# Kernel tuning notes

Measured on AMD Instinct MI355X. Metric: run time of the kernel, lower is better.

The kernel has to match this reference:

```python
import jax, jax.numpy as jnp
import numpy as np
import math

C = 768; H = 12; B = 2; TX = 2048; TC = 2048

def setup_inputs() -> dict:
    key = jax.random.key(0)
    ks = jax.random.split(key, 20)
    w = lambda k, s: jax.random.normal(k, s, dtype=jnp.float32) * 0.02
    inp = {
        "x": jax.random.normal(ks[0], (B, TX, C), dtype=jnp.float32),
        "context": jax.random.normal(ks[1], (B, TC, C), dtype=jnp.float32),
        "ln1_g": jnp.ones((C,), jnp.float32), "ln1_b": jnp.zeros((C,), jnp.float32),
        "ln2_g": jnp.ones((C,), jnp.float32), "ln2_b": jnp.zeros((C,), jnp.float32),
        "ln3_g": jnp.ones((C,), jnp.float32), "ln3_b": jnp.zeros((C,), jnp.float32),
        "sa_wq": w(ks[2], (C, C)), "sa_bq": jnp.zeros((C,), jnp.float32),
        "sa_wk": w(ks[3], (C, C)), "sa_bk": jnp.zeros((C,), jnp.float32),
        "sa_wv": w(ks[4], (C, C)), "sa_bv": jnp.zeros((C,), jnp.float32),
        "sa_wo": w(ks[5], (C, C)), "sa_bo": jnp.zeros((C,), jnp.float32),
        "xa_wq": w(ks[6], (C, C)), "xa_bq": jnp.zeros((C,), jnp.float32),
        "xa_wk": w(ks[7], (C, C)), "xa_bk": jnp.zeros((C,), jnp.float32),
        "xa_wv": w(ks[8], (C, C)), "xa_bv": jnp.zeros((C,), jnp.float32),
        "xa_wo": w(ks[9], (C, C)), "xa_bo": jnp.zeros((C,), jnp.float32),
        "mlp_w1": w(ks[10], (C, 4 * C)), "mlp_b1": jnp.zeros((4 * C,), jnp.float32),
        "mlp_w2": w(ks[11], (4 * C, C)), "mlp_b2": jnp.zeros((C,), jnp.float32),
        "n_head": H,
    }
    return inp

def _layernorm(x, g, b, eps=1e-5):
    mu = jnp.mean(x, axis=-1, keepdims=True)
    var = jnp.mean(jnp.square(x - mu), axis=-1, keepdims=True)
    return (x - mu) * jax.lax.rsqrt(var + eps) * g + b

def _attn(xq, xkv, wq, bq, wk, bk, wv, bv, wo, bo, n_head):
    Bq, Tq, Cm = xq.shape
    Tk = xkv.shape[1]
    dh = Cm // n_head
    q = (xq @ wq + bq).reshape(Bq, Tq, n_head, dh)
    k = (xkv @ wk + bk).reshape(Bq, Tk, n_head, dh)
    v = (xkv @ wv + bv).reshape(Bq, Tk, n_head, dh)
    att = jnp.einsum('bqhd,bkhd->bhqk', q, k) * (1.0 / math.sqrt(dh))
    att = jax.nn.softmax(att, axis=-1)
    y = jnp.einsum('bhqk,bkhd->bqhd', att, v).reshape(Bq, Tq, Cm)
    return y @ wo + bo

def reference(x, context, ln1_g, ln1_b, ln2_g, ln2_b, ln3_g, ln3_b,
              sa_wq, sa_bq, sa_wk, sa_bk, sa_wv, sa_bv, sa_wo, sa_bo,
              xa_wq, xa_bq, xa_wk, xa_bk, xa_wv, xa_bv, xa_wo, xa_bo,
              mlp_w1, mlp_b1, mlp_w2, mlp_b2, n_head):
    # pre-LN residual self-attention
    x = x + _attn(_layernorm(x, ln1_g, ln1_b), _layernorm(x, ln1_g, ln1_b),
                  sa_wq, sa_bq, sa_wk, sa_bk, sa_wv, sa_bv, sa_wo, sa_bo, n_head)
    # pre-LN residual cross-attention (context not normalized, matching source)
    x = x + _attn(_layernorm(x, ln2_g, ln2_b), context,
                  xa_wq, xa_bq, xa_wk, xa_bk, xa_wv, xa_bv, xa_wo, xa_bo, n_head)
    # pre-LN residual MLP with exact (erf) GELU, as torch.nn.GELU default
    h = _layernorm(x, ln3_g, ln3_b)
    x = x + (jax.nn.gelu(h @ mlp_w1 + mlp_b1, approximate=False) @ mlp_w2 + mlp_b2)
    return (x, context)
```

## Files before the change

kernel.cpp:

```cpp
#include <hip/hip_runtime.h>
#include <hip/hip_bf16.h>
#include <math.h>

#define CDIM 768
#define HDIM 3072
#define NROWS 4096
#define TSEQ 2048
#define NHEAD 12
#define KVSPLIT 4
#define KVLEN (TSEQ / KVSPLIT)

typedef unsigned short u16;
typedef unsigned int   u32;
typedef __attribute__((ext_vector_type(8))) short short8;
typedef __attribute__((ext_vector_type(4))) float f32x4;

#define QSCALE 0.18033688011112042f

static __device__ __forceinline__ u16 f2bf(float f) {
    u32 x = __float_as_uint(f);
    x += 0x7fffu + ((x >> 16) & 1u);
    return (u16)(x >> 16);
}
static __device__ __forceinline__ float bf2f(u16 x) {
    return __uint_as_float((u32)x << 16);
}
static __device__ __forceinline__ u32 cvt_pk_bf16(float lo, float hi) {
    u32 r;
    asm("v_cvt_pk_bf16_f32 %0, %1, %2" : "=v"(r) : "v"(lo), "v"(hi));
    return r;
}

#define GLL16(g, l)                                                            \
    __builtin_amdgcn_global_load_lds(                                          \
        (const __attribute__((address_space(1))) void*)(g),                    \
        (__attribute__((address_space(3))) void*)(l), 16, 0, 0)

__launch_bounds__(256)
__global__ void wtrans(const float* __restrict__ w, u16* __restrict__ wt,
                       int K, int N) {
    __shared__ float t[32][33];
    const int n0 = blockIdx.x * 32, k0 = blockIdx.y * 32;
    const int tx = threadIdx.x & 31, ty = threadIdx.x >> 5;
#pragma unroll
    for (int i = ty; i < 32; i += 8)
        t[i][tx] = w[(size_t)(k0 + i) * N + n0 + tx];
    __syncthreads();
#pragma unroll
    for (int i = ty; i < 32; i += 8)
        wt[(size_t)(n0 + i) * K + k0 + tx] = f2bf(t[tx][i]);
}

struct WT4 { const float* w[4]; u16* wt[4]; };
__launch_bounds__(256)
__global__ void wtrans4(WT4 a) {
    __shared__ float t[32][33];
    const float* __restrict__ w = a.w[blockIdx.z];
    u16* __restrict__ wt = a.wt[blockIdx.z];
    const int n0 = blockIdx.x * 32, k0 = blockIdx.y * 32;
    const int tx = threadIdx.x & 31, ty = threadIdx.x >> 5;
#pragma unroll
    for (int i = ty; i < 32; i += 8)
        t[i][tx] = w[(size_t)(k0 + i) * CDIM + n0 + tx];
    __syncthreads();
#pragma unroll
    for (int i = ty; i < 32; i += 8)
        wt[(size_t)(n0 + i) * CDIM + k0 + tx] = f2bf(t[tx][i]);
}

__launch_bounds__(256)
__global__ void cvt_copy(const float* __restrict__ in, u16* __restrict__ out,
                         int n4) {
    int i = blockIdx.x * 256 + threadIdx.x;
    if (i >= n4) return;
    float4 v = ((const float4*)in)[i];
    ushort4 o;
    o.x = f2bf(v.x); o.y = f2bf(v.y); o.z = f2bf(v.z); o.w = f2bf(v.w);
    ((ushort4*)out)[i] = o;
}

__launch_bounds__(256)
__global__ void ln_kernel(const float* __restrict__ x, const float* __restrict__ g,
                          const float* __restrict__ bta, u16* __restrict__ out) {
    const int row = blockIdx.x, tid = threadIdx.x;
    const float* xr = x + (size_t)row * CDIM;
    float v0 = xr[tid], v1 = xr[tid + 256], v2 = xr[tid + 512];
    __shared__ float red[8];
    float s = v0 + v1 + v2;
#pragma unroll
    for (int m = 1; m < 64; m <<= 1) s += __shfl_xor(s, m);
    if ((tid & 63) == 0) red[tid >> 6] = s;
    __syncthreads();
    const float mu = (red[0] + red[1] + red[2] + red[3]) * (1.f / CDIM);
    const float d0 = v0 - mu, d1 = v1 - mu, d2 = v2 - mu;
    float q = d0 * d0 + d1 * d1 + d2 * d2;
#pragma unroll
    for (int m = 1; m < 64; m <<= 1) q += __shfl_xor(q, m);
    if ((tid & 63) == 0) red[4 + (tid >> 6)] = q;
    __syncthreads();
    const float var = (red[4] + red[5] + red[6] + red[7]) * (1.f / CDIM);
    const float rstd = rsqrtf(var + 1e-5f);
    u16* orow = out + (size_t)row * CDIM;
    orow[tid]       = f2bf(d0 * rstd * g[tid]       + bta[tid]);
    orow[tid + 256] = f2bf(d1 * rstd * g[tid + 256] + bta[tid + 256]);
    orow[tid + 512] = f2bf(d2 * rstd * g[tid + 512] + bta[tid + 512]);
}

struct GemmArgs {
    const u16* A[3];
    const u16* BT[3];
    const float* bias[3];
    const float* res[3];
    void* out[3];
    float alpha[3];
    int M, N, K;
};

template <int EPI, int BM, int BN = 128>
__launch_bounds__(256)
__global__ void gemm_bt(GemmArgs ga) {
    constexpr int MF = BM / 32, NF = BN / 32;
    __shared__ u16 Abuf[BM * 32];
    __shared__ u16 Bbuf[BN * 32];
    const int z = blockIdx.z;
    const u16* __restrict__ A  = ga.A[z];
    const u16* __restrict__ BT = ga.BT[z];
    const float* __restrict__ bias = ga.bias[z];
    const float* __restrict__ res  = ga.res[z];
    void* outv = ga.out[z];
    const float alpha = ga.alpha[z];
    const int N = ga.N, K = ga.K;

    const int tid = threadIdx.x;
    const int lane = tid & 63, w = tid >> 6;
    const int m0 = blockIdx.x * BM, n0 = blockIdx.y * BN;
    const int wr = (w >> 1) * (BM / 2), wc = (w & 1) * (BN / 2);
    const int lr = lane & 15, lc = lane >> 4;

    const int srowA = (BM == 128) ? (w * 32 + (lane >> 2)) : (tid >> 2);
    const int srowB = (BN == 128) ? (w * 32 + (lane >> 2)) : (tid >> 2);
    const int scol = (lane & 3) * 8;
    const u16* Ag = A + (size_t)(m0 + srowA) * K + scol;
    const u16* Bg = BT + (size_t)(n0 + srowB) * K + scol;
    char* Ab = (char*)Abuf + w * (BM == 128 ? 2048 : 1024);
    char* Bb = (char*)Bbuf + w * (BN == 128 ? 2048 : 1024);

    f32x4 acc[MF][NF];
#pragma unroll
    for (int m = 0; m < MF; ++m)
#pragma unroll
        for (int n = 0; n < NF; ++n) acc[m][n] = (f32x4){0.f, 0.f, 0.f, 0.f};

    const int nk = K >> 5;
    for (int kt = 0; kt < nk; ++kt) {
        const int ko = kt * 32;
        GLL16(Ag + ko, Ab);
        if constexpr (BM == 128) GLL16(Ag + 16 * K + ko, Ab + 1024);
        GLL16(Bg + ko, Bb);
        if constexpr (BN == 128) GLL16(Bg + 16 * K + ko, Bb + 1024);
        __syncthreads();
        short8 af[MF], bfv[NF];
#pragma unroll
        for (int m = 0; m < MF; ++m)
            af[m] = *(const short8*)((const char*)Abuf +
                                     (size_t)(wr + m * 16 + lr) * 64 + lc * 16);
#pragma unroll
        for (int n = 0; n < NF; ++n)
            bfv[n] = *(const short8*)((const char*)Bbuf +
                                      (size_t)(wc + n * 16 + lr) * 64 + lc * 16);
#pragma unroll
        for (int m = 0; m < MF; ++m)
#pragma unroll
            for (int n = 0; n < NF; ++n)
                acc[m][n] = __builtin_amdgcn_mfma_f32_16x16x32_bf16(
                    af[m], bfv[n], acc[m][n], 0, 0, 0);
        __syncthreads();
    }

#pragma unroll
    for (int n = 0; n < NF; ++n) {
        const int gc = n0 + wc + n * 16 + lr;
        const float bs = bias[gc];
#pragma unroll
        for (int m = 0; m < MF; ++m) {
            const int gr = m0 + wr + m * 16 + lc * 4;
#pragma unroll
            for (int r = 0; r < 4; ++r) {
                float v = (acc[m][n][r] + bs) * alpha;
                const size_t idx = (size_t)(gr + r) * N + gc;
                if constexpr (EPI == 0) {
                    ((u16*)outv)[idx] = f2bf(v);
                } else if constexpr (EPI == 1) {
                    ((float*)outv)[idx] = res[idx] + v;
                } else {
                    float gel = 0.5f * v * (1.0f + erff(v * 0.70710678118654752f));
                    ((u16*)outv)[idx] = f2bf(gel);
                }
            }
        }
    }
}

static __device__ __forceinline__ void softmax_pack(f32x4 sf[4], float& mrow,
                                                    float& lrow, f32x4 oacc[4],
                                                    short8& p0, short8& p1) {
    float pm;
    {
        float a0 = fmaxf(fmaxf(sf[0][0], sf[0][1]), fmaxf(sf[0][2], sf[0][3]));
        float a1 = fmaxf(fmaxf(sf[1][0], sf[1][1]), fmaxf(sf[1][2], sf[1][3]));
        float a2 = fmaxf(fmaxf(sf[2][0], sf[2][1]), fmaxf(sf[2][2], sf[2][3]));
        float a3 = fmaxf(fmaxf(sf[3][0], sf[3][1]), fmaxf(sf[3][2], sf[3][3]));
        pm = fmaxf(fmaxf(a0, a1), fmaxf(a2, a3));
        pm = fmaxf(pm, __shfl_xor(pm, 16));
        pm = fmaxf(pm, __shfl_xor(pm, 32));
    }
    if (!__all(pm <= mrow)) {
        const float mn = fmaxf(mrow, pm);
        const float corr = exp2f(mrow - mn);
        mrow = mn;
        lrow *= corr;
#pragma unroll
        for (int fd = 0; fd < 4; ++fd)
#pragma unroll
            for (int r = 0; r < 4; ++r) oacc[fd][r] *= corr;
    }
#pragma unroll
    for (int fn = 0; fn < 4; ++fn)
#pragma unroll
        for (int r = 0; r < 4; ++r) sf[fn][r] = exp2f(sf[fn][r] - mrow);
    float rs;
    {
        float s0 = (sf[0][0] + sf[0][1]) + (sf[0][2] + sf[0][3]);
        float s1 = (sf[1][0] + sf[1][1]) + (sf[1][2] + sf[1][3]);
        float s2 = (sf[2][0] + sf[2][1]) + (sf[2][2] + sf[2][3]);
        float s3 = (sf[3][0] + sf[3][1]) + (sf[3][2] + sf[3][3]);
        rs = (s0 + s1) + (s2 + s3);
        rs += __shfl_xor(rs, 16);
        rs += __shfl_xor(rs, 32);
    }
    lrow += rs;
    int4 pw0, pw1;
    pw0.x = cvt_pk_bf16(sf[0][0], sf[0][1]);
    pw0.y = cvt_pk_bf16(sf[0][2], sf[0][3]);
    pw0.z = cvt_pk_bf16(sf[1][0], sf[1][1]);
    pw0.w = cvt_pk_bf16(sf[1][2], sf[1][3]);
    pw1.x = cvt_pk_bf16(sf[2][0], sf[2][1]);
    pw1.y = cvt_pk_bf16(sf[2][2], sf[2][3]);
    pw1.z = cvt_pk_bf16(sf[3][0], sf[3][1]);
    pw1.w = cvt_pk_bf16(sf[3][2], sf[3][3]);
    p0 = *(short8*)&pw0;
    p1 = *(short8*)&pw1;
}

__launch_bounds__(256, 4)
__global__ void attn_split(const u16* __restrict__ Qb, const u16* __restrict__ Kb,
                           const u16* __restrict__ Vb, u16* __restrict__ Opart,
                           float2* __restrict__ ml) {
    __shared__ u16 Klds[64 * 72];
    __shared__ u16 Vt[64 * 72];
    const int tid = threadIdx.x;
    const int lane = tid & 63, w = tid >> 6;
    const int lr = lane & 15, lc = lane >> 4;
    const int b = blockIdx.y / NHEAD, h = blockIdx.y % NHEAD;
    const int z = blockIdx.z;
    const size_t qrowA = (size_t)b * TSEQ + blockIdx.x * 128 + w * 16;
    const size_t qrowB = qrowA + 64;
    const size_t krow0 = (size_t)b * TSEQ + (size_t)z * KVLEN;
    const int hc = h * 64;

    short8 qa0, qa1, qb0, qb1;
    {
        const u16* qp = Qb + (qrowA + lr) * CDIM + hc + lc * 8;
        qa0 = *(const short8*)qp;
        qa1 = *(const short8*)(qp + 32);
        const u16* qp2 = Qb + (qrowB + lr) * CDIM + hc + lc * 8;
        qb0 = *(const short8*)qp2;
        qb1 = *(const short8*)(qp2 + 32);
    }
    f32x4 oaccA[4], oaccB[4];
#pragma unroll
    for (int r = 0; r < 4; ++r) {
        oaccA[r] = (f32x4){0.f, 0.f, 0.f, 0.f};
        oaccB[r] = (f32x4){0.f, 0.f, 0.f, 0.f};
    }
    float mA = -3e38f, lA = 0.f, mB = -3e38f, lB = 0.f;

    const int stg_r = tid >> 2, stg_s = tid & 3;
    const u16* kg = Kb + (krow0 + stg_r) * CDIM + hc + stg_s * 16;
    const u16* vg = Vb + (krow0 + stg_r) * CDIM + hc + stg_s * 16;
    uint4 ka0 = *(const uint4*)kg, ka1 = *(const uint4*)(kg + 8);
    uint4 va0 = *(const uint4*)vg, va1 = *(const uint4*)(vg + 8);
    const int sig = ((stg_r >> 5) << 5) + (((stg_r >> 2) & 3) << 3) +
                    (((stg_r >> 4) & 1) << 2) + (stg_r & 3);
    char* vdst = (char*)Vt + ((2 * sig) ^ (stg_s << 5)) +
                 (size_t)(stg_s * 16) * 144;

    for (int kt = 0; kt < KVLEN / 64; ++kt) {
        __syncthreads();
        {
            *(uint4*)&Klds[stg_r * 72 + stg_s * 16]     = ka0;
            *(uint4*)&Klds[stg_r * 72 + stg_s * 16 + 8] = ka1;
            u16 tmp[16];
            *(uint4*)(tmp)     = va0;
            *(uint4*)(tmp + 8) = va1;
#pragma unroll
            for (int j = 0; j < 16; ++j)
                *(u16*)(vdst + (size_t)j * 144) = tmp[j];
        }
        if (kt < KVLEN / 64 - 1) {
            kg += 64 * CDIM; vg += 64 * CDIM;
            ka0 = *(const uint4*)kg; ka1 = *(const uint4*)(kg + 8);
            va0 = *(const uint4*)vg; va1 = *(const uint4*)(vg + 8);
        }
        __syncthreads();

        f32x4 sfA[4], sfB[4];
#pragma unroll
        for (int fn = 0; fn < 4; ++fn) {
            const u16* kr = &Klds[(lr + fn * 16) * 72 + lc * 8];
            short8 kb0 = *(const short8*)kr;
            short8 kb1 = *(const short8*)(kr + 32);
            f32x4 t = (f32x4){0.f, 0.f, 0.f, 0.f};
            t = __builtin_amdgcn_mfma_f32_16x16x32_bf16(kb0, qa0, t, 0, 0, 0);
            t = __builtin_amdgcn_mfma_f32_16x16x32_bf16(kb1, qa1, t, 0, 0, 0);
            sfA[fn] = t;
            f32x4 u = (f32x4){0.f, 0.f, 0.f, 0.f};
            u = __builtin_amdgcn_mfma_f32_16x16x32_bf16(kb0, qb0, u, 0, 0, 0);
            u = __builtin_amdgcn_mfma_f32_16x16x32_bf16(kb1, qb1, u, 0, 0, 0);
            sfB[fn] = u;
        }

        short8 pA0, pA1, pB0, pB1;
        softmax_pack(sfA, mA, lA, oaccA, pA0, pA1);
        softmax_pack(sfB, mB, lB, oaccB, pB0, pB1);

#pragma unroll
        for (int fd = 0; fd < 4; ++fd) {
            const char* vtb = (const char*)Vt + (size_t)(lr + fd * 16) * 144;
            short8 vb0 = *(const short8*)(vtb + ((lc * 16) ^ (fd * 32)));
            short8 vb1 = *(const short8*)(vtb + ((lc * 16 + 64) ^ (fd * 32)));
            oaccA[fd] = __builtin_amdgcn_mfma_f32_16x16x32_bf16(vb0, pA0, oaccA[fd], 0, 0, 0);
            oaccA[fd] = __builtin_amdgcn_mfma_f32_16x16x32_bf16(vb1, pA1, oaccA[fd], 0, 0, 0);
            oaccB[fd] = __builtin_amdgcn_mfma_f32_16x16x32_bf16(vb0, pB0, oaccB[fd], 0, 0, 0);
            oaccB[fd] = __builtin_amdgcn_mfma_f32_16x16x32_bf16(vb1, pB1, oaccB[fd], 0, 0, 0);
        }
    }

    u16* oA = Opart + (size_t)z * NROWS * CDIM + (qrowA + lr) * CDIM + hc + lc * 4;
    u16* oB = Opart + (size_t)z * NROWS * CDIM + (qrowB + lr) * CDIM + hc + lc * 4;
#pragma unroll
    for (int fd = 0; fd < 4; ++fd) {
        ushort4 o;
        o.x = f2bf(oaccA[fd][0]); o.y = f2bf(oaccA[fd][1]);
        o.z = f2bf(oaccA[fd][2]); o.w = f2bf(oaccA[fd][3]);
        *(ushort4*)(oA + fd * 16) = o;
        o.x = f2bf(oaccB[fd][0]); o.y = f2bf(oaccB[fd][1]);
        o.z = f2bf(oaccB[fd][2]); o.w = f2bf(oaccB[fd][3]);
        *(ushort4*)(oB + fd * 16) = o;
    }
    if (lc == 0) {
        ml[((size_t)z * NROWS + qrowA + lr) * NHEAD + h] = (float2){mA, lA};
        ml[((size_t)z * NROWS + qrowB + lr) * NHEAD + h] = (float2){mB, lB};
    }
}

__launch_bounds__(256)
__global__ void attn_merge4(const u16* __restrict__ P, const float2* __restrict__ ml,
                            u16* __restrict__ out) {
    const int i4 = blockIdx.x * 256 + threadIdx.x;
    const size_t base = (size_t)i4 * 4;
    const int row = (int)(base / CDIM);
    const int head = (int)(base - (size_t)row * CDIM) >> 6;
    float2 a[KVSPLIT];
    float M = -3e38f;
#pragma unroll
    for (int z = 0; z < KVSPLIT; ++z) {
        a[z] = ml[((size_t)z * NROWS + row) * NHEAD + head];
        M = fmaxf(M, a[z].x);
    }
    float den = 0.f, e[KVSPLIT];
#pragma unroll
    for (int z = 0; z < KVSPLIT; ++z) {
        e[z] = exp2f(a[z].x - M);
        den += a[z].y * e[z];
    }
    const float rden = 1.f / den;
    float o0 = 0.f, o1 = 0.f, o2 = 0.f, o3 = 0.f;
#pragma unroll
    for (int z = 0; z < KVSPLIT; ++z) {
        ushort4 p = *(const ushort4*)(P + (size_t)z * NROWS * CDIM + base);
        o0 += bf2f(p.x) * e[z];
        o1 += bf2f(p.y) * e[z];
        o2 += bf2f(p.z) * e[z];
        o3 += bf2f(p.w) * e[z];
    }
    ushort4 o;
    o.x = f2bf(o0 * rden); o.y = f2bf(o1 * rden);
    o.z = f2bf(o2 * rden); o.w = f2bf(o3 * rden);
    *(ushort4*)(out + base) = o;
}

extern "C" void kernel_launch(void* const* d_in, const int* in_sizes, int n_in,
                              void* d_out, int out_size, void* d_ws, size_t ws_size,
                              hipStream_t stream) {
    const float* x     = (const float*)d_in[0];
    const float* ctx   = (const float*)d_in[1];
    const float* ln1g  = (const float*)d_in[2];
    const float* ln1b  = (const float*)d_in[3];
    const float* ln2g  = (const float*)d_in[4];
    const float* ln2b  = (const float*)d_in[5];
    const float* ln3g  = (const float*)d_in[6];
    const float* ln3b  = (const float*)d_in[7];
    const float* sa_wq = (const float*)d_in[8];
    const float* sa_bq = (const float*)d_in[9];
    const float* sa_wk = (const float*)d_in[10];
    const float* sa_bk = (const float*)d_in[11];
    const float* sa_wv = (const float*)d_in[12];
    const float* sa_bv = (const float*)d_in[13];
    const float* sa_wo = (const float*)d_in[14];
    const float* sa_bo = (const float*)d_in[15];
    const float* xa_wq = (const float*)d_in[16];
    const float* xa_bq = (const float*)d_in[17];
    const float* xa_wk = (const float*)d_in[18];
    const float* xa_bk = (const float*)d_in[19];
    const float* xa_wv = (const float*)d_in[20];
    const float* xa_bv = (const float*)d_in[21];
    const float* xa_wo = (const float*)d_in[22];
    const float* xa_bo = (const float*)d_in[23];
    const float* m_w1  = (const float*)d_in[24];
    const float* m_b1  = (const float*)d_in[25];
    const float* m_w2  = (const float*)d_in[26];
    const float* m_b2  = (const float*)d_in[27];

    float* out_x   = (float*)d_out;
    float* out_ctx = out_x + (size_t)NROWS * CDIM;
    u16* Opart = (u16*)d_out;

    const size_t SZ_ACT  = (size_t)NROWS * CDIM * 2;
    const size_t SZ_WBIG = (size_t)HDIM * CDIM * 2;
    const size_t SZ_R    = (size_t)NROWS * CDIM * 4;
    const size_t NEEDED  = 5 * SZ_ACT + SZ_R + SZ_WBIG;
    if (ws_size < NEEDED) return;

    char* ws = (char*)d_ws;
    u16* qb    = (u16*)(ws);
    u16* kb    = (u16*)(ws + 1 * SZ_ACT);
    u16* vb    = (u16*)(ws + 2 * SZ_ACT);
    u16* ctxb  = (u16*)(ws + 3 * SZ_ACT);
    u16* hb    = qb;
    u16* lnbuf = (u16*)(ws + 4 * SZ_ACT);
    u16* attB  = lnbuf;
    float* R   = (float*)(ws + 5 * SZ_ACT);
    u16* Wq    = (u16*)(ws + 5 * SZ_ACT + SZ_R);
    u16* Wk    = Wq + (size_t)CDIM * CDIM;
    u16* Wv    = Wk + (size_t)CDIM * CDIM;
    u16* Wo    = Wv + (size_t)CDIM * CDIM;
    float2* ml = (float2*)Wq;

    const dim3 tb(256);
    GemmArgs ga;
    WT4 wg;

    cvt_copy<<<dim3(3072), tb, 0, stream>>>(ctx, ctxb, NROWS * CDIM / 4);

    ln_kernel<<<dim3(NROWS), tb, 0, stream>>>(x, ln1g, ln1b, lnbuf);
    wg.w[0] = sa_wq; wg.w[1] = sa_wk; wg.w[2] = sa_wv; wg.w[3] = sa_wo;
    wg.wt[0] = Wq;   wg.wt[1] = Wk;   wg.wt[2] = Wv;   wg.wt[3] = Wo;
    wtrans4<<<dim3(24, 24, 4), tb, 0, stream>>>(wg);
    ga = GemmArgs{};
    ga.A[0] = lnbuf; ga.BT[0] = Wq; ga.bias[0] = sa_bq; ga.out[0] = qb; ga.alpha[0] = QSCALE;
    ga.A[1] = lnbuf; ga.BT[1] = Wk; ga.bias[1] = sa_bk; ga.out[1] = kb; ga.alpha[1] = 1.f;
    ga.A[2] = lnbuf; ga.BT[2] = Wv; ga.bias[2] = sa_bv; ga.out[2] = vb; ga.alpha[2] = 1.f;
    ga.M = 4096; ga.N = 768; ga.K = 768;
    gemm_bt<0, 128><<<dim3(32, 6, 3), tb, 0, stream>>>(ga);
    attn_split<<<dim3(16, 24, KVSPLIT), tb, 0, stream>>>(qb, kb, vb, Opart, ml);
    attn_merge4<<<dim3(NROWS * CDIM / 1024), tb, 0, stream>>>(Opart, ml, attB);
    ga = GemmArgs{};
    ga.A[0] = attB; ga.BT[0] = Wo; ga.bias[0] = sa_bo; ga.res[0] = x; ga.out[0] = R; ga.alpha[0] = 1.f;
    ga.M = 4096; ga.N = 768; ga.K = 768;
    gemm_bt<1, 64, 64><<<dim3(64, 12, 1), tb, 0, stream>>>(ga);

    ln_kernel<<<dim3(NROWS), tb, 0, stream>>>(R, ln2g, ln2b, lnbuf);
    wg.w[0] = xa_wq; wg.w[1] = xa_wk; wg.w[2] = xa_wv; wg.w[3] = xa_wo;
    wg.wt[0] = Wq;   wg.wt[1] = Wk;   wg.wt[2] = Wv;   wg.wt[3] = Wo;
    wtrans4<<<dim3(24, 24, 4), tb, 0, stream>>>(wg);
    ga = GemmArgs{};
    ga.A[0] = lnbuf; ga.BT[0] = Wq; ga.bias[0] = xa_bq; ga.out[0] = qb; ga.alpha[0] = QSCALE;
    ga.A[1] = ctxb;  ga.BT[1] = Wk; ga.bias[1] = xa_bk; ga.out[1] = kb; ga.alpha[1] = 1.f;
    ga.A[2] = ctxb;  ga.BT[2] = Wv; ga.bias[2] = xa_bv; ga.out[2] = vb; ga.alpha[2] = 1.f;
    ga.M = 4096; ga.N = 768; ga.K = 768;
    gemm_bt<0, 128><<<dim3(32, 6, 3), tb, 0, stream>>>(ga);
    attn_split<<<dim3(16, 24, KVSPLIT), tb, 0, stream>>>(qb, kb, vb, Opart, ml);
    attn_merge4<<<dim3(NROWS * CDIM / 1024), tb, 0, stream>>>(Opart, ml, attB);
    hipMemcpyAsync(out_ctx, ctx, (size_t)NROWS * CDIM * 4,
                   hipMemcpyDeviceToDevice, stream);
    ga = GemmArgs{};
    ga.A[0] = attB; ga.BT[0] = Wo; ga.bias[0] = xa_bo; ga.res[0] = R; ga.out[0] = R; ga.alpha[0] = 1.f;
    ga.M = 4096; ga.N = 768; ga.K = 768;
    gemm_bt<1, 64, 64><<<dim3(64, 12, 1), tb, 0, stream>>>(ga);

    ln_kernel<<<dim3(NROWS), tb, 0, stream>>>(R, ln3g, ln3b, lnbuf);
    wtrans<<<dim3(96, 24), tb, 0, stream>>>(m_w1, Wq, 768, 3072);
    ga = GemmArgs{};
    ga.A[0] = lnbuf; ga.BT[0] = Wq; ga.bias[0] = m_b1; ga.out[0] = hb; ga.alpha[0] = 1.f;
    ga.M = 4096; ga.N = 3072; ga.K = 768;
    gemm_bt<2, 128><<<dim3(32, 24, 1), tb, 0, stream>>>(ga);
    wtrans<<<dim3(24, 96), tb, 0, stream>>>(m_w2, Wq, 3072, 768);
    ga = GemmArgs{};
    ga.A[0] = hb; ga.BT[0] = Wq; ga.bias[0] = m_b2; ga.res[0] = R; ga.out[0] = out_x; ga.alpha[0] = 1.f;
    ga.M = 4096; ga.N = 768; ga.K = 3072;
    gemm_bt<1, 64, 64><<<dim3(64, 12, 1), tb, 0, stream>>>(ga);

    (void)in_sizes; (void)n_in; (void)out_size;
}
```

Baseline: 340.7 us.

## Merge layernorm, conversions and weight transposes into combined prologue kernels

Replaces the separate cvt_copy, ln_kernel and weight-transpose launches before each stage with one kernel per stage that dispatches on block index, which removes several launches and lets the independent pieces overlap. The W2 transpose now goes to the output context area as scratch, so it can be done up front, and the context memcpy moves to the very end. The QKV GEMMs also switch to a narrower 128x64 tile with twice as many blocks. Costs are branch divergence across block roles and reuse of the output buffer as scratch before the final copy.

```diff
diff --git a/kernel.cpp b/kernel.cpp
--- a/kernel.cpp
+++ b/kernel.cpp
@@ -36,56 +36,22 @@
         (const __attribute__((address_space(1))) void*)(g),                    \
         (__attribute__((address_space(3))) void*)(l), 16, 0, 0)
 
-__launch_bounds__(256)
-__global__ void wtrans(const float* __restrict__ w, u16* __restrict__ wt,
-                       int K, int N) {
-    __shared__ float t[32][33];
-    const int n0 = blockIdx.x * 32, k0 = blockIdx.y * 32;
-    const int tx = threadIdx.x & 31, ty = threadIdx.x >> 5;
-#pragma unroll
-    for (int i = ty; i < 32; i += 8)
-        t[i][tx] = w[(size_t)(k0 + i) * N + n0 + tx];
-    __syncthreads();
-#pragma unroll
-    for (int i = ty; i < 32; i += 8)
-        wt[(size_t)(n0 + i) * K + k0 + tx] = f2bf(t[tx][i]);
-}
-
-struct WT4 { const float* w[4]; u16* wt[4]; };
-__launch_bounds__(256)
-__global__ void wtrans4(WT4 a) {
-    __shared__ float t[32][33];
-    const float* __restrict__ w = a.w[blockIdx.z];
-    u16* __restrict__ wt = a.wt[blockIdx.z];
-    const int n0 = blockIdx.x * 32, k0 = blockIdx.y * 32;
-    const int tx = threadIdx.x & 31, ty = threadIdx.x >> 5;
-#pragma unroll
-    for (int i = ty; i < 32; i += 8)
-        t[i][tx] = w[(size_t)(k0 + i) * CDIM + n0 + tx];
-    __syncthreads();
-#pragma unroll
-    for (int i = ty; i < 32; i += 8)
-        wt[(size_t)(n0 + i) * CDIM + k0 + tx] = f2bf(t[tx][i]);
-}
-
-__launch_bounds__(256)
-__global__ void cvt_copy(const float* __restrict__ in, u16* __restrict__ out,
-                         int n4) {
-    int i = blockIdx.x * 256 + threadIdx.x;
-    if (i >= n4) return;
+static __device__ void do_cvt(int blk, const float* __restrict__ in,
+                              u16* __restrict__ out) {
+    const int i = blk * 256 + threadIdx.x;
     float4 v = ((const float4*)in)[i];
     ushort4 o;
     o.x = f2bf(v.x); o.y = f2bf(v.y); o.z = f2bf(v.z); o.w = f2bf(v.w);
     ((ushort4*)out)[i] = o;
 }
 
-__launch_bounds__(256)
-__global__ void ln_kernel(const float* __restrict__ x, const float* __restrict__ g,
-                          const float* __restrict__ bta, u16* __restrict__ out) {
-    const int row = blockIdx.x, tid = threadIdx.x;
+static __device__ void do_ln(int row, const float* __restrict__ x,
+                             const float* __restrict__ g,
+                             const float* __restrict__ bta,
+                             u16* __restrict__ out, float* red) {
+    const int tid = threadIdx.x;
     const float* xr = x + (size_t)row * CDIM;
     float v0 = xr[tid], v1 = xr[tid + 256], v2 = xr[tid + 512];
-    __shared__ float red[8];
     float s = v0 + v1 + v2;
 #pragma unroll
     for (int m = 1; m < 64; m <<= 1) s += __shfl_xor(s, m);
@@ -104,6 +70,66 @@
     orow[tid]       = f2bf(d0 * rstd * g[tid]       + bta[tid]);
     orow[tid + 256] = f2bf(d1 * rstd * g[tid + 256] + bta[tid + 256]);
     orow[tid + 512] = f2bf(d2 * rstd * g[tid + 512] + bta[tid + 512]);
+}
+
+static __device__ void do_wt(int bx, int by, const float* __restrict__ w,
+                             u16* __restrict__ wt, int K, int N, float* t ) {
+    const int n0 = bx * 32, k0 = by * 32;
+    const int tx = threadIdx.x & 31, ty = threadIdx.x >> 5;
+#pragma unroll
+    for (int i = ty; i < 32; i += 8)
+        t[i * 33 + tx] = w[(size_t)(k0 + i) * N + n0 + tx];
+    __syncthreads();
+#pragma unroll
+    for (int i = ty; i < 32; i += 8)
+        wt[(size_t)(n0 + i) * K + k0 + tx] = f2bf(t[tx * 33 + i]);
+}
+
+struct Pre1 {
+    const float* ctx; u16* ctxb;
+    const float* x; const float* g; const float* bta; u16* lnout;
+    const float* w[4]; u16* wt[4];
+};
+__launch_bounds__(256)
+__global__ void pre1_kernel(Pre1 p) {
+    __shared__ float smem[32 * 33];
+    int bid = blockIdx.x;
+    if (bid < 3072) { do_cvt(bid, p.ctx, p.ctxb); return; }
+    bid -= 3072;
+    if (bid < 4096) { do_ln(bid, p.x, p.g, p.bta, p.lnout, smem); return; }
+    bid -= 4096;
+    const int z = bid / 576, rem = bid % 576;
+    do_wt(rem % 24, rem / 24, p.w[z], p.wt[z], CDIM, CDIM, smem);
+}
+
+struct Pre2 {
+    const float* x; const float* g; const float* bta; u16* lnout;
+    const float* w[4]; u16* wt[4];
+};
+__launch_bounds__(256)
+__global__ void pre2_kernel(Pre2 p) {
+    __shared__ float smem[32 * 33];
+    int bid = blockIdx.x;
+    if (bid < 4096) { do_ln(bid, p.x, p.g, p.bta, p.lnout, smem); return; }
+    bid -= 4096;
+    const int z = bid / 576, rem = bid % 576;
+    do_wt(rem % 24, rem / 24, p.w[z], p.wt[z], CDIM, CDIM, smem);
+}
+
+struct Pre3 {
+    const float* x; const float* g; const float* bta; u16* lnout;
+    const float* w1; u16* wt1;
+    const float* w2; u16* wt2;
+};
+__launch_bounds__(256)
+__global__ void pre3_kernel(Pre3 p) {
+    __shared__ float smem[32 * 33];
+    int bid = blockIdx.x;
+    if (bid < 4096) { do_ln(bid, p.x, p.g, p.bta, p.lnout, smem); return; }
+    bid -= 4096;
+    if (bid < 2304) { do_wt(bid % 96, bid / 96, p.w1, p.wt1, CDIM, HDIM, smem); return; }
+    bid -= 2304;
+    do_wt(bid % 24, bid / 24, p.w2, p.wt2, HDIM, CDIM, smem);
 }
 
 struct GemmArgs {
@@ -435,6 +461,7 @@
     float* out_x   = (float*)d_out;
     float* out_ctx = out_x + (size_t)NROWS * CDIM;
     u16* Opart = (u16*)d_out;
+    u16* W2s   = (u16*)out_ctx;
 
     const size_t SZ_ACT  = (size_t)NROWS * CDIM * 2;
     const size_t SZ_WBIG = (size_t)HDIM * CDIM * 2;
@@ -459,20 +486,19 @@
 
     const dim3 tb(256);
     GemmArgs ga;
-    WT4 wg;
-
-    cvt_copy<<<dim3(3072), tb, 0, stream>>>(ctx, ctxb, NROWS * CDIM / 4);
-
-    ln_kernel<<<dim3(NROWS), tb, 0, stream>>>(x, ln1g, ln1b, lnbuf);
-    wg.w[0] = sa_wq; wg.w[1] = sa_wk; wg.w[2] = sa_wv; wg.w[3] = sa_wo;
-    wg.wt[0] = Wq;   wg.wt[1] = Wk;   wg.wt[2] = Wv;   wg.wt[3] = Wo;
-    wtrans4<<<dim3(24, 24, 4), tb, 0, stream>>>(wg);
+
+    Pre1 p1;
+    p1.ctx = ctx; p1.ctxb = ctxb;
+    p1.x = x; p1.g = ln1g; p1.bta = ln1b; p1.lnout = lnbuf;
+    p1.w[0] = sa_wq; p1.w[1] = sa_wk; p1.w[2] = sa_wv; p1.w[3] = sa_wo;
+    p1.wt[0] = Wq;   p1.wt[1] = Wk;   p1.wt[2] = Wv;   p1.wt[3] = Wo;
+    pre1_kernel<<<dim3(3072 + 4096 + 2304), tb, 0, stream>>>(p1);
     ga = GemmArgs{};
     ga.A[0] = lnbuf; ga.BT[0] = Wq; ga.bias[0] = sa_bq; ga.out[0] = qb; ga.alpha[0] = QSCALE;
     ga.A[1] = lnbuf; ga.BT[1] = Wk; ga.bias[1] = sa_bk; ga.out[1] = kb; ga.alpha[1] = 1.f;
     ga.A[2] = lnbuf; ga.BT[2] = Wv; ga.bias[2] = sa_bv; ga.out[2] = vb; ga.alpha[2] = 1.f;
     ga.M = 4096; ga.N = 768; ga.K = 768;
-    gemm_bt<0, 128><<<dim3(32, 6, 3), tb, 0, stream>>>(ga);
+    gemm_bt<0, 128, 64><<<dim3(32, 12, 3), tb, 0, stream>>>(ga);
     attn_split<<<dim3(16, 24, KVSPLIT), tb, 0, stream>>>(qb, kb, vb, Opart, ml);
     attn_merge4<<<dim3(NROWS * CDIM / 1024), tb, 0, stream>>>(Opart, ml, attB);
     ga = GemmArgs{};
@@ -480,36 +506,39 @@
     ga.M = 4096; ga.N = 768; ga.K = 768;
     gemm_bt<1, 64, 64><<<dim3(64, 12, 1), tb, 0, stream>>>(ga);
 
-    ln_kernel<<<dim3(NROWS), tb, 0, stream>>>(R, ln2g, ln2b, lnbuf);
-    wg.w[0] = xa_wq; wg.w[1] = xa_wk; wg.w[2] = xa_wv; wg.w[3] = xa_wo;
-    wg.wt[0] = Wq;   wg.wt[1] = Wk;   wg.wt[2] = Wv;   wg.wt[3] = Wo;
-    wtrans4<<<dim3(24, 24, 4), tb, 0, stream>>>(wg);
+    Pre2 p2;
+    p2.x = R; p2.g = ln2g; p2.bta = ln2b; p2.lnout = lnbuf;
+    p2.w[0] = xa_wq; p2.w[1] = xa_wk; p2.w[2] = xa_wv; p2.w[3] = xa_wo;
+    p2.wt[0] = Wq;   p2.wt[1] = Wk;   p2.wt[2] = Wv;   p2.wt[3] = Wo;
+    pre2_kernel<<<dim3(4096 + 2304), tb, 0, stream>>>(p2);
     ga = GemmArgs{};
     ga.A[0] = lnbuf; ga.BT[0] = Wq; ga.bias[0] = xa_bq; ga.out[0] = qb; ga.alpha[0] = QSCALE;
     ga.A[1] = ctxb;  ga.BT[1] = Wk; ga.bias[1] = xa_bk; ga.out[1] = kb; ga.alpha[1] = 1.f;
     ga.A[2] = ctxb;  ga.BT[2] = Wv; ga.bias[2] = xa_bv; ga.out[2] = vb; ga.alpha[2] = 1.f;
     ga.M = 4096; ga.N = 768; ga.K = 768;
-    gemm_bt<0, 128><<<dim3(32, 6, 3), tb, 0, stream>>>(ga);
+    gemm_bt<0, 128, 64><<<dim3(32, 12, 3), tb, 0, stream>>>(ga);
     attn_split<<<dim3(16, 24, KVSPLIT), tb, 0, stream>>>(qb, kb, vb, Opart, ml);
     attn_merge4<<<dim3(NROWS * CDIM / 1024), tb, 0, stream>>>(Opart, ml, attB);
-    hipMemcpyAsync(out_ctx, ctx, (size_t)NROWS * CDIM * 4,
-                   hipMemcpyDeviceToDevice, stream);
     ga = GemmArgs{};
     ga.A[0] = attB; ga.BT[0] = Wo; ga.bias[0] = xa_bo; ga.res[0] = R; ga.out[0] = R; ga.alpha[0] = 1.f;
     ga.M = 4096; ga.N = 768; ga.K = 768;
     gemm_bt<1, 64, 64><<<dim3(64, 12, 1), tb, 0, stream>>>(ga);
 
-    ln_kernel<<<dim3(NROWS), tb, 0, stream>>>(R, ln3g, ln3b, lnbuf);
-    wtrans<<<dim3(96, 24), tb, 0, stream>>>(m_w1, Wq, 768, 3072);
+    Pre3 p3;
+    p3.x = R; p3.g = ln3g; p3.bta = ln3b; p3.lnout = lnbuf;
+    p3.w1 = m_w1; p3.wt1 = Wq;
+    p3.w2 = m_w2; p3.wt2 = W2s;
+    pre3_kernel<<<dim3(4096 + 2304 + 2304), tb, 0, stream>>>(p3);
     ga = GemmArgs{};
     ga.A[0] = lnbuf; ga.BT[0] = Wq; ga.bias[0] = m_b1; ga.out[0] = hb; ga.alpha[0] = 1.f;
     ga.M = 4096; ga.N = 3072; ga.K = 768;
     gemm_bt<2, 128><<<dim3(32, 24, 1), tb, 0, stream>>>(ga);
-    wtrans<<<dim3(24, 96), tb, 0, stream>>>(m_w2, Wq, 3072, 768);
     ga = GemmArgs{};
-    ga.A[0] = hb; ga.BT[0] = Wq; ga.bias[0] = m_b2; ga.res[0] = R; ga.out[0] = out_x; ga.alpha[0] = 1.f;
+    ga.A[0] = hb; ga.BT[0] = W2s; ga.bias[0] = m_b2; ga.res[0] = R; ga.out[0] = out_x; ga.alpha[0] = 1.f;
     ga.M = 4096; ga.N = 768; ga.K = 3072;
     gemm_bt<1, 64, 64><<<dim3(64, 12, 1), tb, 0, stream>>>(ga);
+    hipMemcpyAsync(out_ctx, ctx, (size_t)NROWS * CDIM * 4,
+                   hipMemcpyDeviceToDevice, stream);
 
     (void)in_sizes; (void)n_in; (void)out_size;
 }
```

Measured after the change: 337.9 us. About the same (-0.8%).
